# Kernel optimization log

Measured on AMD Instinct MI355X. Metric: run time of the kernel, lower is better.

## Reference

```python
import jax, jax.numpy as jnp
import numpy as np
from jax import lax

B, T, K, HID, NCLS = 32, 2048, 17, 64, 10
DILATIONS = (1, 1, 2)
RESIDUAL = (False, True, True)
TK = 3  # temporal kernel
BN_EPS = 1e-5
LN_EPS = 1e-5

COCO_EDGES = [(0,1),(0,2),(1,3),(2,4),(5,6),(5,7),(7,9),(6,8),(8,10),(5,11),(6,12),(11,13),(13,15),(12,14),(14,16)]

def build_skeleton_adj(num_kpts=K):
    adj = np.eye(num_kpts, dtype=np.float32)
    for i, j in COCO_EDGES:
        adj[i, j] = 1.0
        adj[j, i] = 1.0
    adj = adj + np.eye(num_kpts, dtype=np.float32)
    deg = adj.sum(axis=1, keepdims=True)
    deg[deg == 0] = 1.0
    return adj / deg

def setup_inputs() -> dict:
    key = jax.random.key(0)
    ks = jax.random.split(key, 8)
    kpts = jax.random.normal(ks[0], (B, T, K, 3), dtype=jnp.float32)
    adj = jnp.asarray(build_skeleton_adj(K))
    gcn_w0 = jax.random.normal(ks[1], (3, HID), dtype=jnp.float32) * (1.0 / np.sqrt(3))
    gcn_w1 = jax.random.normal(ks[2], (HID, HID), dtype=jnp.float32) * (1.0 / np.sqrt(HID))
    gcn_w2 = jax.random.normal(ks[3], (HID, HID), dtype=jnp.float32) * (1.0 / np.sqrt(HID))
    tcn_w = jax.random.normal(ks[4], (3, HID, HID, TK, 1), dtype=jnp.float32) * (1.0 / np.sqrt(HID * TK))
    bn_scale = 1.0 + 0.1 * jax.random.normal(ks[5], (3, HID), dtype=jnp.float32)
    bn_bias = 0.1 * jax.random.normal(ks[6], (3, HID), dtype=jnp.float32)
    bn_mean = 0.1 * jax.random.normal(ks[7], (3, HID), dtype=jnp.float32)
    bn_var = 0.5 + jax.random.uniform(jax.random.fold_in(key, 7), (3, HID), dtype=jnp.float32)
    ln_scale = jnp.ones((HID,), dtype=jnp.float32)
    ln_bias = jnp.zeros((HID,), dtype=jnp.float32)
    fc_w = jax.random.normal(jax.random.fold_in(key, 8), (HID, NCLS), dtype=jnp.float32) * (1.0 / np.sqrt(HID))
    fc_b = jnp.zeros((NCLS,), dtype=jnp.float32)
    return dict(kpts=kpts, adj=adj, gcn_w0=gcn_w0, gcn_w1=gcn_w1, gcn_w2=gcn_w2,
                tcn_w=tcn_w, bn_scale=bn_scale, bn_bias=bn_bias, bn_mean=bn_mean,
                bn_var=bn_var, ln_scale=ln_scale, ln_bias=ln_bias, fc_w=fc_w, fc_b=fc_b)

def _stgn_block(x, adj, gw, tw, bs, bb, bm, bv, dilation, residual):
    # x: [B, C_in, T, K]
    y = jnp.einsum('bctk,kv->bctv', x, adj)          # graph conv over keypoints
    y = jnp.einsum('bitk,io->botk', y, gw)           # channel mixing (intended GCN weight)
    pad = (TK - 1) * dilation // 2
    y = lax.conv_general_dilated(y, tw, window_strides=(1, 1),
                                 padding=[(pad, pad), (0, 0)],
                                 rhs_dilation=(dilation, 1),
                                 dimension_numbers=('NCHW', 'OIHW', 'NCHW'))
    inv = (bs / jnp.sqrt(bv + BN_EPS))[None, :, None, None]
    y = y * inv + (bb - bs * bm / jnp.sqrt(bv + BN_EPS))[None, :, None, None]
    y = jax.nn.relu(y)
    if residual:
        y = y + x
    return y

def reference(kpts, adj, gcn_w0, gcn_w1, gcn_w2, tcn_w, bn_scale, bn_bias, bn_mean,
              bn_var, ln_scale, ln_bias, fc_w, fc_b):
    x = jnp.transpose(kpts, (0, 3, 1, 2))  # [B, 3, T, K]
    gws = (gcn_w0, gcn_w1, gcn_w2)
    for i in range(3):
        x = _stgn_block(x, adj, gws[i], tcn_w[i], bn_scale[i], bn_bias[i],
                        bn_mean[i], bn_var[i], DILATIONS[i], RESIDUAL[i])
    feat = x.mean(axis=(2, 3))  # [B, HID] temporal/spatial mean pool
    mu = feat.mean(axis=-1, keepdims=True)
    var = feat.var(axis=-1, keepdims=True)
    feat = (feat - mu) / jnp.sqrt(var + LN_EPS) * ln_scale + ln_bias
    return feat @ fc_w + fc_b  # [B, NCLS]
```

## Files before the change

### kernel.cpp

```cpp
#include <hip/hip_runtime.h>
#include <hip/hip_bf16.h>
#include <math.h>

#define T_DIM 2048
#define K_DIM 17
#define HID   64
#define B_DIM 32

typedef short s16x8 __attribute__((ext_vector_type(8)));
typedef unsigned u32x2 __attribute__((ext_vector_type(2)));
typedef float f32x4 __attribute__((ext_vector_type(4)));

__device__ __forceinline__ float bf2f(short u) {
    unsigned v = ((unsigned)(unsigned short)u) << 16;
    return __builtin_bit_cast(float, v);
}
__device__ __forceinline__ short f2bf(float f) {
    __hip_bfloat16 h = __float2bfloat16(f);
    return __builtin_bit_cast(short, h);
}
__device__ __forceinline__ short f2bf_fast(float f) {
    unsigned u = __builtin_bit_cast(unsigned, f);
    return (short)((u + 0x8000u) >> 16);
}
__device__ __forceinline__ unsigned pk2bf(float lo, float hi) {
    unsigned ul = __builtin_bit_cast(unsigned, lo);
    unsigned uh = __builtin_bit_cast(unsigned, hi);
    return ((ul + 0x8000u) >> 16) | ((uh + 0x8000u) & 0xFFFF0000u);
}

static constexpr int NBR_PTR[18] = {0,3,6,9,11,13,17,21,24,27,29,31,34,37,40,43,45,47};
static constexpr int NBR_K[47] = {
    0,1,2,  0,1,3,  0,2,4,  1,3,  2,4,
    5,6,7,11,  5,6,8,12,  5,7,9,  6,8,10,  7,9,  8,10,
    5,11,13,  6,12,14,  11,13,15,  12,14,16,  13,15,  14,16 };
__device__ const int d_NBR_PTR[18] = {0,3,6,9,11,13,17,21,24,27,29,31,34,37,40,43,45,47};
__device__ const int d_NBR_K[47] = {
    0,1,2,  0,1,3,  0,2,4,  1,3,  2,4,
    5,6,7,11,  5,6,8,12,  5,7,9,  6,8,10,  7,9,  8,10,
    5,11,13,  6,12,14,  11,13,15,  12,14,16,  13,15,  14,16 };

__global__ void fold_weights_kernel(
    const float* __restrict__ gw0, const float* __restrict__ gw1,
    const float* __restrict__ gw2, const float* __restrict__ tcn,
    const float* __restrict__ bns, const float* __restrict__ bnb,
    const float* __restrict__ bnm, const float* __restrict__ bnv,
    short* __restrict__ effT0, short* __restrict__ effT12,
    float* __restrict__ bnc)
{
    int tid = blockIdx.x * blockDim.x + threadIdx.x;
    int stride = gridDim.x * blockDim.x;
    for (int idx = tid; idx < 2048; idx += stride) {
        int o = idx >> 5, k = idx & 31, dt = k >> 3, cin = k & 7;
        float s = 0.f;
        if (dt < 3 && cin < 3)
            for (int m = 0; m < 64; m++)
                s += gw0[cin * 64 + m] * tcn[(o * 64 + m) * 3 + dt];
        effT0[idx] = f2bf(s);
    }
    for (int idx = tid; idx < 24576; idx += stride) {
        int blk = idx / 12288;
        int r = idx - blk * 12288;
        int o = r / 192, k = r - o * 192, dt = k >> 6, c = k & 63;
        const float* gw = blk ? gw2 : gw1;
        const float* tw = tcn + (size_t)(blk + 1) * 64 * 64 * 3;
        float s = 0.f;
        for (int m = 0; m < 64; m++)
            s += gw[c * 64 + m] * tw[(o * 64 + m) * 3 + dt];
        effT12[idx] = f2bf(s);
    }
    for (int i = tid; i < 192; i += stride) {
        float inv = bns[i] * rsqrtf(bnv[i] + 1e-5f);
        bnc[i] = inv;
        bnc[192 + i] = bnb[i] - bnm[i] * inv;
    }
}

__global__ __launch_bounds__(256, 4) void stgcn_ab_kernel(
    const float* __restrict__ x, const float* __restrict__ adj,
    const short* __restrict__ effT0, const short* __restrict__ effT12,
    const float* __restrict__ bnc, short* __restrict__ y2)
{
    __shared__ float adj_s[289];
    __shared__ __align__(16) float xt[12 * 51];
    __shared__ __align__(16) float xtg[12 * 51];
    __shared__ __align__(16) short ybuf[170 * 72];

    const int tid = threadIdx.x;
    const int b = blockIdx.y;
    const int t0 = blockIdx.x * 8;
    const int lane = tid & 63, wave = tid >> 6;
    const int col = lane & 15, kgrp = lane >> 4;

    for (int i = tid; i < 289; i += 256) adj_s[i] = adj[i];
    {
        const int tbase = t0 - 2;
        const float* xb = x + (size_t)(b * T_DIM + tbase) * 51;
        for (int i = tid; i < 612; i += 256) {
            int tt = tbase + i / 51;
            xt[i] = (tt >= 0 && tt < T_DIM) ? xb[i] : 0.f;
        }
    }
    s16x8 af1 = *(const s16x8*)(effT0 + (wave * 16 + col) * 32 + kgrp * 8);
    s16x8 af2[6];
    #pragma unroll
    for (int kk = 0; kk < 6; kk++)
        af2[kk] = *(const s16x8*)(effT12 +
            (wave * 16 + col) * 192 + kk * 32 + kgrp * 8);
    __syncthreads();

    for (int it = tid; it < 612; it += 256) {
        const int u = it / 51;
        const int rem = it - u * 51;
        const int j = rem / 3, c = rem - j * 3;
        float acc = 0.f;
        const int p0 = d_NBR_PTR[j], p1 = d_NBR_PTR[j + 1];
        for (int e = p0; e < p1; e++) {
            int k = d_NBR_K[e];
            acc += adj_s[k * 17 + j] * xt[u * 51 + k * 3 + c];
        }
        xtg[it] = acc;
    }
    __syncthreads();

    {
        f32x4 inv4 = *(const f32x4*)&bnc[wave * 16 + kgrp * 4];
        f32x4 sh4  = *(const f32x4*)&bnc[192 + wave * 16 + kgrp * 4];
        for (int tile = 0; tile < 11; tile++) {
            const int r = tile * 16 + col;
            const int me = r < 170 ? r : 169;
            const int s = (me * 241) >> 12;
            const int j = me - s * 17;
            s16x8 bfr = (s16x8){0,0,0,0,0,0,0,0};
            if (kgrp < 3) {
                const float* xp = &xtg[(s + kgrp) * 51 + j * 3];
                bfr[0] = f2bf_fast(xp[0]);
                bfr[1] = f2bf_fast(xp[1]);
                bfr[2] = f2bf_fast(xp[2]);
            }
            f32x4 acc = __builtin_amdgcn_mfma_f32_16x16x32_bf16(
                af1, bfr, (f32x4){0.f, 0.f, 0.f, 0.f}, 0, 0, 0);
            const int t = t0 - 1 + s;
            const bool valid = (t >= 0) && (t < T_DIM);
            if (r < 170) {
                float v0 = valid ? fmaxf(acc[0] * inv4[0] + sh4[0], 0.f) : 0.f;
                float v1 = valid ? fmaxf(acc[1] * inv4[1] + sh4[1], 0.f) : 0.f;
                float v2 = valid ? fmaxf(acc[2] * inv4[2] + sh4[2], 0.f) : 0.f;
                float v3 = valid ? fmaxf(acc[3] * inv4[3] + sh4[3], 0.f) : 0.f;
                u32x2 st; st[0] = pk2bf(v0, v1); st[1] = pk2bf(v2, v3);
                *(u32x2*)&ybuf[r * 72 + wave * 16 + kgrp * 4] = st;
            }
        }
    }
    __syncthreads();

    f32x4 acc2[9];
    #pragma unroll
    for (int t2 = 0; t2 < 9; t2++) acc2[t2] = (f32x4){0.f, 0.f, 0.f, 0.f};
    #pragma unroll
    for (int kk = 0; kk < 6; kk++) {
        #pragma unroll
        for (int t2 = 0; t2 < 9; t2++) {
            const int r = t2 * 16 + col;
            const int me = r < 136 ? r : 135;
            s16x8 bfr = *(const s16x8*)&ybuf[
                (me + 17 * (kk >> 1)) * 72 + (kk & 1) * 32 + kgrp * 8];
            acc2[t2] = __builtin_amdgcn_mfma_f32_16x16x32_bf16(
                af2[kk], bfr, acc2[t2], 0, 0, 0);
        }
    }
    unsigned rv[17];
    {
        const int tl = tid >> 5, o0 = (tid & 31) * 2;
        #pragma unroll
        for (int v = 0; v < 17; v++)
            rv[v] = *(const unsigned*)&ybuf[((tl + 1) * 17 + v) * 72 + o0];
    }
    __syncthreads();

    #pragma unroll
    for (int t2 = 0; t2 < 9; t2++) {
        const int r = t2 * 16 + col;
        if (r < 136) {
            u32x2 st;
            st[0] = pk2bf(acc2[t2][0], acc2[t2][1]);
            st[1] = pk2bf(acc2[t2][2], acc2[t2][3]);
            *(u32x2*)&ybuf[r * 72 + wave * 16 + kgrp * 4] = st;
        }
    }
    __syncthreads();

    {
        const int tl = tid >> 5, o0 = (tid & 31) * 2;
        const float inv0 = bnc[64 + o0], inv1 = bnc[64 + o0 + 1];
        const float sh0 = bnc[256 + o0], sh1 = bnc[256 + o0 + 1];
        float zk0[17], zk1[17];
        #pragma unroll
        for (int k = 0; k < 17; k++) {
            unsigned u = *(const unsigned*)&ybuf[(tl * 17 + k) * 72 + o0];
            zk0[k] = bf2f((short)(u & 0xFFFF));
            zk1[k] = bf2f((short)(u >> 16));
        }
        const size_t gout = ((size_t)(b * T_DIM + t0 + tl) * K_DIM) * 64;
        #pragma unroll
        for (int v = 0; v < 17; v++) {
            float g0 = 0.f, g1 = 0.f;
            #pragma unroll
            for (int e = NBR_PTR[v]; e < NBR_PTR[v + 1]; e++) {
                int k = NBR_K[e];
                float w = adj_s[k * 17 + v];
                g0 += w * zk0[k]; g1 += w * zk1[k];
            }
            float v0 = fmaxf(g0 * inv0 + sh0, 0.f) + bf2f((short)(rv[v] & 0xFFFF));
            float v1 = fmaxf(g1 * inv1 + sh1, 0.f) + bf2f((short)(rv[v] >> 16));
            *(unsigned*)&y2[gout + (size_t)v * 64 + o0] = pk2bf(v0, v1);
        }
    }
}

__global__ __launch_bounds__(256, 4) void stgcn_c_kernel(
    const short* __restrict__ y2, const float* __restrict__ adj,
    const short* __restrict__ effW3, const float* __restrict__ bnc,
    float* __restrict__ part, int b0)
{
    __shared__ float adj_s[289];
    __shared__ __align__(16) short ybuf[204 * 72];

    float* pr = (float*)&ybuf[136 * 72];

    const int tid = threadIdx.x;
    const int b = blockIdx.y;
    const int t0 = blockIdx.x * 8;
    const int lane = tid & 63, wave = tid >> 6;
    const int col = lane & 15, kgrp = lane >> 4;

    for (int i = tid; i < 289; i += 256) adj_s[i] = adj[i];
    s16x8 af3[6];
    #pragma unroll
    for (int kk = 0; kk < 6; kk++)
        af3[kk] = *(const s16x8*)(effW3 +
            (wave * 16 + col) * 192 + kk * 32 + kgrp * 8);

    {
        const int bLo = b * (T_DIM * 17);
        const int bHi = bLo + T_DIM * 17;
        const int g0r = bLo + (t0 - 2) * 17;
        for (int idx = tid; idx < 1632; idx += 256) {
            const int row = idx >> 3, c = idx & 7;
            const int gr = g0r + row;
            s16x8 v = (s16x8){0,0,0,0,0,0,0,0};
            if (gr >= bLo && gr < bHi)
                v = *(const s16x8*)(y2 + (size_t)gr * 64 + c * 8);
            *(s16x8*)&ybuf[row * 72 + c * 8] = v;
        }
    }
    __syncthreads();

    f32x4 acc3[9];
    #pragma unroll
    for (int t3 = 0; t3 < 9; t3++) acc3[t3] = (f32x4){0.f, 0.f, 0.f, 0.f};
    #pragma unroll
    for (int kk = 0; kk < 6; kk++) {
        #pragma unroll
        for (int t3 = 0; t3 < 9; t3++) {
            const int r = t3 * 16 + col;
            const int me = r < 136 ? r : 135;
            s16x8 bfr = *(const s16x8*)&ybuf[
                (me + 34 * (kk >> 1)) * 72 + (kk & 1) * 32 + kgrp * 8];
            acc3[t3] = __builtin_amdgcn_mfma_f32_16x16x32_bf16(
                af3[kk], bfr, acc3[t3], 0, 0, 0);
        }
    }
    float rs0 = 0.f, rs1 = 0.f;
    {
        const int tl = tid >> 5, o0 = (tid & 31) * 2;
        #pragma unroll
        for (int v = 0; v < 17; v++) {
            unsigned u = *(const unsigned*)&ybuf[((tl + 2) * 17 + v) * 72 + o0];
            rs0 += bf2f((short)(u & 0xFFFF));
            rs1 += bf2f((short)(u >> 16));
        }
    }
    __syncthreads();

    #pragma unroll
    for (int t3 = 0; t3 < 9; t3++) {
        const int r = t3 * 16 + col;
        if (r < 136) {
            u32x2 st;
            st[0] = pk2bf(acc3[t3][0], acc3[t3][1]);
            st[1] = pk2bf(acc3[t3][2], acc3[t3][3]);
            *(u32x2*)&ybuf[r * 72 + wave * 16 + kgrp * 4] = st;
        }
    }
    __syncthreads();

    {
        const int tl = tid >> 5, o0 = (tid & 31) * 2;
        const float inv0 = bnc[128 + o0], inv1 = bnc[128 + o0 + 1];
        const float sh0 = bnc[320 + o0], sh1 = bnc[320 + o0 + 1];
        float zk0[17], zk1[17];
        #pragma unroll
        for (int k = 0; k < 17; k++) {
            unsigned u = *(const unsigned*)&ybuf[(tl * 17 + k) * 72 + o0];
            zk0[k] = bf2f((short)(u & 0xFFFF));
            zk1[k] = bf2f((short)(u >> 16));
        }
        float ps0 = rs0, ps1 = rs1;
        #pragma unroll
        for (int v = 0; v < 17; v++) {
            float g0 = 0.f, g1 = 0.f;
            #pragma unroll
            for (int e = NBR_PTR[v]; e < NBR_PTR[v + 1]; e++) {
                int k = NBR_K[e];
                float w = adj_s[k * 17 + v];
                g0 += w * zk0[k]; g1 += w * zk1[k];
            }
            ps0 += fmaxf(g0 * inv0 + sh0, 0.f);
            ps1 += fmaxf(g1 * inv1 + sh1, 0.f);
        }
        *(float2*)&pr[tl * 64 + o0] = make_float2(ps0, ps1);
    }
    __syncthreads();
    if (tid < 64) {
        float s = 0.f;
        #pragma unroll
        for (int i = 0; i < 8; i++) s += pr[i * 64 + tid];
        part[((size_t)(b0 + b) * 256 + blockIdx.x) * 64 + tid] = s;
    }
}

__global__ __launch_bounds__(256) void finish_kernel(
    const float* __restrict__ part, const float* __restrict__ ln_s,
    const float* __restrict__ ln_b, const float* __restrict__ fc_w,
    const float* __restrict__ fc_b, float* __restrict__ out)
{
    __shared__ float red[4][64];
    __shared__ float ns[64];
    const int b = blockIdx.x;
    const int g = threadIdx.x >> 6, c = threadIdx.x & 63;
    float s = 0.f;
    for (int j = 0; j < 64; j++)
        s += part[((size_t)b * 256 + g * 64 + j) * 64 + c];
    red[g][c] = s;
    __syncthreads();
    if (threadIdx.x < 64) {
        float feat = (red[0][c] + red[1][c] + red[2][c] + red[3][c])
                   / (float)(T_DIM * K_DIM);
        float m = feat;
        #pragma unroll
        for (int off = 32; off > 0; off >>= 1) m += __shfl_down(m, off);
        m = __shfl(m, 0) / 64.f;
        float d = feat - m;
        float v = d * d;
        #pragma unroll
        for (int off = 32; off > 0; off >>= 1) v += __shfl_down(v, off);
        v = __shfl(v, 0) / 64.f;
        ns[c] = d * rsqrtf(v + 1e-5f) * ln_s[c] + ln_b[c];
    }
    __syncthreads();
    if (threadIdx.x < 10) {
        float o = fc_b[threadIdx.x];
        for (int i = 0; i < 64; i++) o += ns[i] * fc_w[i * 10 + threadIdx.x];
        out[b * 10 + threadIdx.x] = o;
    }
}

extern "C" void kernel_launch(void* const* d_in, const int* in_sizes, int n_in,
                              void* d_out, int out_size, void* d_ws, size_t ws_size,
                              hipStream_t stream)
{
    const float* kpts = (const float*)d_in[0];
    const float* adj  = (const float*)d_in[1];
    const float* gw0  = (const float*)d_in[2];
    const float* gw1  = (const float*)d_in[3];
    const float* gw2  = (const float*)d_in[4];
    const float* tcn  = (const float*)d_in[5];
    const float* bns  = (const float*)d_in[6];
    const float* bnb  = (const float*)d_in[7];
    const float* bnm  = (const float*)d_in[8];
    const float* bnv  = (const float*)d_in[9];
    const float* lns  = (const float*)d_in[10];
    const float* lnb  = (const float*)d_in[11];
    const float* fcw  = (const float*)d_in[12];
    const float* fcb  = (const float*)d_in[13];
    float* out = (float*)d_out;

    float* bnc  = (float*)d_ws;
    float* part = bnc + 384;
    short* effT0  = (short*)(part + (size_t)B_DIM * 256 * 64);
    short* effT12 = effT0 + 2048;
    short* y2     = effT12 + 24576;
    const size_t fixed_bytes = 384 * 4 + (size_t)B_DIM * 256 * 64 * 4
                             + 2048 * 2 + 24576 * 2;
    const size_t y_per_b = (size_t)T_DIM * K_DIM * 64 * 2;

    int cb = B_DIM;
    while (cb > 1 && fixed_bytes + (size_t)cb * y_per_b > ws_size) cb >>= 1;

    fold_weights_kernel<<<64, 256, 0, stream>>>(gw0, gw1, gw2, tcn,
                                                bns, bnb, bnm, bnv,
                                                effT0, effT12, bnc);

    for (int b0 = 0; b0 < B_DIM; b0 += cb) {
        stgcn_ab_kernel<<<dim3(T_DIM / 8, cb), 256, 0, stream>>>(
            kpts + (size_t)b0 * T_DIM * K_DIM * 3, adj, effT0, effT12, bnc, y2);
        stgcn_c_kernel<<<dim3(T_DIM / 8, cb), 256, 0, stream>>>(
            y2, adj, effT12 + 12288, bnc, part, b0);
    }

    finish_kernel<<<B_DIM, 256, 0, stream>>>(part, lns, lnb, fcw, fcb, out);
}
```

Before: 265.6 us.

## Precompute graph-mixed input in separate kernel and pad y2 to drop bounds checks

Adds a premix kernel that applies the adjacency mixing to the raw keypoints once per (b,t,j) and writes a time-padded, 52-float-stride buffer. The stage-A kernel then copies this tile with float4 loads instead of loading raw input and recomputing the mix for halo rows. It also removes one block barrier. y2 gets two zero-padded time steps on each side so the stage-C load can skip its per-row bounds checks. The cost is an extra kernel launch and extra global traffic for the intermediate buffer, plus a larger workspace, which could shrink the batch chunk size.

Result: faster. 241.3 us (-9.2%).

```diff
diff --git a/kernel.cpp b/kernel.cpp
--- a/kernel.cpp
+++ b/kernel.cpp
@@ -3,6 +3,7 @@
 #include <math.h>
 
 #define T_DIM 2048
+#define TP_DIM 2052
 #define K_DIM 17
 #define HID   64
 #define B_DIM 32
@@ -76,14 +77,50 @@
     }
 }
 
+__global__ __launch_bounds__(256) void premix_kernel(
+    const float* __restrict__ x, const float* __restrict__ adj,
+    float* __restrict__ xg, short* __restrict__ y2, int cb)
+{
+    const int idx = blockIdx.x * 256 + threadIdx.x;
+    const int total = cb * TP_DIM * K_DIM;
+    if (idx < total) {
+        const int b = idx / (TP_DIM * K_DIM);
+        const int rem = idx - b * (TP_DIM * K_DIM);
+        const int tp = rem / K_DIM, j = rem - tp * K_DIM;
+        const int t = tp - 2;
+        float a0 = 0.f, a1 = 0.f, a2 = 0.f;
+        if (t >= 0 && t < T_DIM) {
+            const float* xp = x + ((size_t)b * T_DIM + t) * 51;
+            const int p0 = d_NBR_PTR[j], p1 = d_NBR_PTR[j + 1];
+            for (int e = p0; e < p1; e++) {
+                int k = d_NBR_K[e];
+                float w = adj[k * 17 + j];
+                a0 += w * xp[k * 3 + 0];
+                a1 += w * xp[k * 3 + 1];
+                a2 += w * xp[k * 3 + 2];
+            }
+        }
+        float* op = xg + ((size_t)b * TP_DIM + tp) * 52 + j * 3;
+        op[0] = a0; op[1] = a1; op[2] = a2;
+    }
+    const int zn = cb * 4 * 1088;
+    for (int z = idx; z < zn; z += gridDim.x * 256) {
+        int bb = z / (4 * 1088);
+        int rr = z - bb * 4 * 1088;
+        int pi = rr / 1088;
+        int ci = rr - pi * 1088;
+        int tp = (pi < 2) ? pi : (2048 + pi);
+        y2[((size_t)(bb * TP_DIM + tp) * K_DIM) * 64 + ci] = 0;
+    }
+}
+
 __global__ __launch_bounds__(256, 4) void stgcn_ab_kernel(
-    const float* __restrict__ x, const float* __restrict__ adj,
+    const float* __restrict__ xg, const float* __restrict__ adj,
     const short* __restrict__ effT0, const short* __restrict__ effT12,
     const float* __restrict__ bnc, short* __restrict__ y2)
 {
     __shared__ float adj_s[289];
-    __shared__ __align__(16) float xt[12 * 51];
-    __shared__ __align__(16) float xtg[12 * 51];
+    __shared__ __align__(16) float xtg[12 * 52];
     __shared__ __align__(16) short ybuf[170 * 72];
 
     const int tid = threadIdx.x;
@@ -94,12 +131,9 @@
 
     for (int i = tid; i < 289; i += 256) adj_s[i] = adj[i];
     {
-        const int tbase = t0 - 2;
-        const float* xb = x + (size_t)(b * T_DIM + tbase) * 51;
-        for (int i = tid; i < 612; i += 256) {
-            int tt = tbase + i / 51;
-            xt[i] = (tt >= 0 && tt < T_DIM) ? xb[i] : 0.f;
-        }
+        const float4* src = (const float4*)(xg + ((size_t)b * TP_DIM + t0) * 52);
+        float4* dst = (float4*)xtg;
+        for (int i = tid; i < 156; i += 256) dst[i] = src[i];
     }
     s16x8 af1 = *(const s16x8*)(effT0 + (wave * 16 + col) * 32 + kgrp * 8);
     s16x8 af2[6];
@@ -107,20 +141,6 @@
     for (int kk = 0; kk < 6; kk++)
         af2[kk] = *(const s16x8*)(effT12 +
             (wave * 16 + col) * 192 + kk * 32 + kgrp * 8);
-    __syncthreads();
-
-    for (int it = tid; it < 612; it += 256) {
-        const int u = it / 51;
-        const int rem = it - u * 51;
-        const int j = rem / 3, c = rem - j * 3;
-        float acc = 0.f;
-        const int p0 = d_NBR_PTR[j], p1 = d_NBR_PTR[j + 1];
-        for (int e = p0; e < p1; e++) {
-            int k = d_NBR_K[e];
-            acc += adj_s[k * 17 + j] * xt[u * 51 + k * 3 + c];
-        }
-        xtg[it] = acc;
-    }
     __syncthreads();
 
     {
@@ -133,7 +153,7 @@
             const int j = me - s * 17;
             s16x8 bfr = (s16x8){0,0,0,0,0,0,0,0};
             if (kgrp < 3) {
-                const float* xp = &xtg[(s + kgrp) * 51 + j * 3];
+                const float* xp = &xtg[(s + kgrp) * 52 + j * 3];
                 bfr[0] = f2bf_fast(xp[0]);
                 bfr[1] = f2bf_fast(xp[1]);
                 bfr[2] = f2bf_fast(xp[2]);
@@ -201,7 +221,7 @@
             zk0[k] = bf2f((short)(u & 0xFFFF));
             zk1[k] = bf2f((short)(u >> 16));
         }
-        const size_t gout = ((size_t)(b * T_DIM + t0 + tl) * K_DIM) * 64;
+        const size_t gout = ((size_t)b * TP_DIM + t0 + tl + 2) * K_DIM * 64;
         #pragma unroll
         for (int v = 0; v < 17; v++) {
             float g0 = 0.f, g1 = 0.f;
@@ -242,16 +262,11 @@
             (wave * 16 + col) * 192 + kk * 32 + kgrp * 8);
 
     {
-        const int bLo = b * (T_DIM * 17);
-        const int bHi = bLo + T_DIM * 17;
-        const int g0r = bLo + (t0 - 2) * 17;
+        const short* base = y2 + ((size_t)b * TP_DIM + t0) * K_DIM * 64;
         for (int idx = tid; idx < 1632; idx += 256) {
             const int row = idx >> 3, c = idx & 7;
-            const int gr = g0r + row;
-            s16x8 v = (s16x8){0,0,0,0,0,0,0,0};
-            if (gr >= bLo && gr < bHi)
-                v = *(const s16x8*)(y2 + (size_t)gr * 64 + c * 8);
-            *(s16x8*)&ybuf[row * 72 + c * 8] = v;
+            *(s16x8*)&ybuf[row * 72 + c * 8] =
+                *(const s16x8*)(base + (size_t)row * 64 + c * 8);
         }
     }
     __syncthreads();
@@ -390,21 +405,28 @@
     float* part = bnc + 384;
     short* effT0  = (short*)(part + (size_t)B_DIM * 256 * 64);
     short* effT12 = effT0 + 2048;
-    short* y2     = effT12 + 24576;
+    float* xg     = (float*)(effT12 + 24576);
     const size_t fixed_bytes = 384 * 4 + (size_t)B_DIM * 256 * 64 * 4
                              + 2048 * 2 + 24576 * 2;
-    const size_t y_per_b = (size_t)T_DIM * K_DIM * 64 * 2;
+    const size_t xg_per_b = (size_t)TP_DIM * 52 * 4;
+    const size_t y2_per_b = (size_t)TP_DIM * K_DIM * 64 * 2;
 
     int cb = B_DIM;
-    while (cb > 1 && fixed_bytes + (size_t)cb * y_per_b > ws_size) cb >>= 1;
+    while (cb > 1 &&
+           fixed_bytes + (size_t)cb * (xg_per_b + y2_per_b) > ws_size)
+        cb >>= 1;
+    short* y2 = (short*)(xg + (size_t)cb * TP_DIM * 52);
 
     fold_weights_kernel<<<64, 256, 0, stream>>>(gw0, gw1, gw2, tcn,
                                                 bns, bnb, bnm, bnv,
                                                 effT0, effT12, bnc);
 
+    const int pm_blocks = (cb * TP_DIM * K_DIM + 255) / 256;
     for (int b0 = 0; b0 < B_DIM; b0 += cb) {
+        premix_kernel<<<pm_blocks, 256, 0, stream>>>(
+            kpts + (size_t)b0 * T_DIM * K_DIM * 3, adj, xg, y2, cb);
         stgcn_ab_kernel<<<dim3(T_DIM / 8, cb), 256, 0, stream>>>(
-            kpts + (size_t)b0 * T_DIM * K_DIM * 3, adj, effT0, effT12, bnc, y2);
+            xg, adj, effT0, effT12, bnc, y2);
         stgcn_c_kernel<<<dim3(T_DIM / 8, cb), 256, 0, stream>>>(
             y2, adj, effT12 + 12288, bnc, part, b0);
     }
```
